# Performance work log

Hardware: AMD Instinct MI355X
Metric: run time of the kernel (lower is better)

Reference implementation:

```python
import jax, jax.numpy as jnp
import numpy as np

T = 2048
D_IN = 1024
D_OUT = 1024
N_HEAD = 16
HEAD_DIM = D_OUT // N_HEAD


def setup_inputs() -> dict:
    key = jax.random.key(0)
    kx, kq, kk, kv = jax.random.split(key, 4)
    s = 1.0 / np.sqrt(D_IN)
    return {
        "x": jax.random.normal(kx, (T, D_IN), dtype=jnp.float32),
        "W_q": jax.random.normal(kq, (D_OUT, D_IN), dtype=jnp.float32) * s,
        "W_k": jax.random.normal(kk, (D_OUT, D_IN), dtype=jnp.float32) * s,
        "W_v": jax.random.normal(kv, (D_OUT, D_IN), dtype=jnp.float32) * s,
    }


def reference(x, W_q, W_k, W_v):
    t = x.shape[0]
    # linear projections (torch Linear: y = x @ W.T), split into heads: [H, T, Dh]
    q = (x @ W_q.T).reshape(t, N_HEAD, HEAD_DIM).transpose(1, 0, 2)
    k = (x @ W_k.T).reshape(t, N_HEAD, HEAD_DIM).transpose(1, 0, 2)
    v = (x @ W_v.T).reshape(t, N_HEAD, HEAD_DIM).transpose(1, 0, 2)
    # raw scores [H, T, T]
    omega = jnp.einsum("hqd,hkd->hqk", q, k)
    causal = jnp.triu(jnp.ones((t, t), dtype=bool), k=1)
    omega = jnp.where(causal[None, :, :], -jnp.inf, omega)
    # NOTE: faithful to source quirk — divides by head_dim**(-0.5),
    # i.e. multiplies scores by sqrt(head_dim)
    att_w = jax.nn.softmax(omega * (HEAD_DIM ** 0.5), axis=-1)
    context = jnp.einsum("hqk,hkd->hqd", att_w, v)  # [H, T, Dh]
    return context.transpose(1, 0, 2).reshape(t, D_OUT)
```

## Files before the change

### kernel.cpp

```cpp
#include <hip/hip_runtime.h>
#include <hip/hip_bf16.h>


typedef __bf16 bf16x8 __attribute__((ext_vector_type(8)));
typedef __bf16 bf16x4 __attribute__((ext_vector_type(4)));
typedef float  f32x4  __attribute__((ext_vector_type(4)));
typedef float  f32x16 __attribute__((ext_vector_type(16)));
typedef unsigned int u32;
typedef u32 u32x2 __attribute__((ext_vector_type(2)));
typedef u32 u32x4 __attribute__((ext_vector_type(4)));

#define MFMA(a, b, c) __builtin_amdgcn_mfma_f32_16x16x32_bf16((a), (b), (c), 0, 0, 0)
#define MFMA32(a, b, c) __builtin_amdgcn_mfma_f32_32x32x16_bf16((a), (b), (c), 0, 0, 0)

#if __has_builtin(__builtin_amdgcn_exp2f)
#define EXP2F(x) __builtin_amdgcn_exp2f(x)
#else
#define EXP2F(x) exp2f(x)
#endif

constexpr int T = 2048, DIN = 1024, DOUT = 1024, NH = 16, DH = 64;
constexpr float SC = 11.5415603f;
constexpr float DEFER = 0.6931472f;

constexpr size_t SZ_XMAT = (size_t)T * DIN * 2;
constexpr size_t SZ_WMAT = (size_t)DOUT * DIN * 2;
constexpr size_t OFF_XH = 0;
constexpr size_t OFF_XL = OFF_XH + SZ_XMAT;
constexpr size_t OFF_QH = OFF_XL + SZ_XMAT;
constexpr size_t OFF_QL = OFF_QH + SZ_XMAT;
constexpr size_t OFF_KH = OFF_QL + SZ_XMAT;
constexpr size_t OFF_KL = OFF_KH + SZ_XMAT;
constexpr size_t OFF_VT = OFF_KL + SZ_XMAT;
constexpr size_t OFF_W  = OFF_VT + SZ_XMAT;

__device__ __forceinline__ void gload_lds16(const void* g, void* l) {
  __builtin_amdgcn_global_load_lds(
      (const __attribute__((address_space(1))) void*)g,
      (__attribute__((address_space(3))) void*)l, 16, 0, 0);
}

__device__ __forceinline__ float xor32f(float x, int hi) {
#if __has_builtin(__builtin_amdgcn_permlane32_swap)
  const u32 xu = __builtin_bit_cast(u32, x);
  const u32x2 rp = __builtin_amdgcn_permlane32_swap(xu, xu, false, false);
  return __builtin_bit_cast(float, hi ? rp[0] : rp[1]);
#else
  return __shfl_xor(x, 32, 64);
#endif
}

__global__ void split_all(const float* __restrict__ x, const float* __restrict__ wq,
                          const float* __restrict__ wk, const float* __restrict__ wv,
                          char* __restrict__ ws) {
  const int i = blockIdx.x * 256 + threadIdx.x;
  const float* src;
  __bf16 *hi, *lo;
  int off;
  if (i < T * DIN / 4) {
    src = x; off = i;
    hi = (__bf16*)(ws + OFF_XH);
    lo = (__bf16*)(ws + OFF_XL);
  } else {
    const int j = i - T * DIN / 4;
    const int z = j >> 18;
    off = j & 262143;
    src = (z == 0) ? wq : ((z == 1) ? wk : wv);
    hi = (__bf16*)(ws + OFF_W + (size_t)z * 2 * SZ_WMAT);
    lo = hi + (size_t)DOUT * DIN;
  }
  const f32x4 v = ((const f32x4*)src)[off];
  bf16x4 h, l;
#pragma unroll
  for (int j = 0; j < 4; ++j) {
    const float xv = v[j];
    const __bf16 hh = (__bf16)xv;
    h[j] = hh;
    l[j] = (__bf16)(xv - (float)hh);
  }
  ((bf16x4*)hi)[off] = h;
  ((bf16x4*)lo)[off] = l;
}

template <bool SPLIT>
__device__ __forceinline__ void proj_loop(const __bf16* __restrict__ Ah,
                                          const __bf16* __restrict__ Al,
                                          const __bf16* __restrict__ Bh,
                                          const __bf16* __restrict__ Bl,
                                          __bf16* lds, int tm, int tn, int lane,
                                          int wv, f32x4 (&acc)[4][4]) {
  constexpr int BUF = SPLIT ? 16384 : 8192;
  constexpr int BOFF = SPLIT ? 8192 : 4096;
  const int wm = wv >> 1, wn = wv & 1;
  const int q4 = lane >> 4, r16 = lane & 15;

  auto STAGE = [&](int ks, int buf) {
    const int k0 = ks * 32;
    __bf16* base = lds + buf * BUF;
#pragma unroll
    for (int j = 0; j < 2; ++j) {
      const int cbase = wv * 128 + j * 64;
      const int cidx = cbase + lane;
      const int row = cidx & 127, kc = cidx >> 7;
      const size_t ga = (size_t)(tm + row) * DIN + k0 + kc * 8;
      const size_t gb = (size_t)(tn + row) * DIN + k0 + kc * 8;
      gload_lds16(Ah + ga, base + cbase * 8);
      gload_lds16(Bh + gb, base + BOFF + cbase * 8);
      if constexpr (SPLIT) {
        gload_lds16(Al + ga, base + 4096 + cbase * 8);
        gload_lds16(Bl + gb, base + 12288 + cbase * 8);
      }
    }
  };

  STAGE(0, 0);
  STAGE(1, 1);

  for (int ks = 0; ks < 32; ++ks) {
    const int buf = ks & 1;
    if (ks < 31) {
      if constexpr (SPLIT) asm volatile("s_waitcnt vmcnt(8)" ::: "memory");
      else                 asm volatile("s_waitcnt vmcnt(4)" ::: "memory");
    } else {
      asm volatile("s_waitcnt vmcnt(0)" ::: "memory");
    }
    __builtin_amdgcn_s_barrier();
    __builtin_amdgcn_sched_barrier(0);

    const __bf16* ldsA = lds + buf * BUF;
    const __bf16* ldsB = ldsA + BOFF;

    bf16x8 fah[4], fbh[4], fal[4], fbl[4];
#pragma unroll
    for (int b = 0; b < 4; ++b) {
      const int ra = wm * 64 + b * 16 + r16;
      const int rb = wn * 64 + b * 16 + r16;
      fah[b] = *(const bf16x8*)(ldsA + (q4 * 128 + ra) * 8);
      fbh[b] = *(const bf16x8*)(ldsB + (q4 * 128 + rb) * 8);
      if constexpr (SPLIT) {
        fal[b] = *(const bf16x8*)(ldsA + 4096 + (q4 * 128 + ra) * 8);
        fbl[b] = *(const bf16x8*)(ldsB + 4096 + (q4 * 128 + rb) * 8);
      }
    }
    __builtin_amdgcn_s_setprio(1);
#pragma unroll
    for (int bm = 0; bm < 4; ++bm)
#pragma unroll
      for (int bn = 0; bn < 4; ++bn) {
        acc[bm][bn] = MFMA(fah[bm], fbh[bn], acc[bm][bn]);
        if constexpr (SPLIT) {
          acc[bm][bn] = MFMA(fah[bm], fbl[bn], acc[bm][bn]);
          acc[bm][bn] = MFMA(fal[bm], fbh[bn], acc[bm][bn]);
        }
      }
    __builtin_amdgcn_s_setprio(0);
    asm volatile("s_waitcnt lgkmcnt(0)" ::: "memory");
    __builtin_amdgcn_sched_barrier(0);
    __builtin_amdgcn_s_barrier();
    __builtin_amdgcn_sched_barrier(0);
    if (ks < 30) STAGE(ks + 2, buf);
  }
}

__global__ __launch_bounds__(256, 2) void qkv_proj(char* ws) {
  const int bid = blockIdx.x;
  const int z = bid >> 7;
  const int t_ = bid & 127;
  const int tm = (t_ >> 3) * 128;
  const int tn = (t_ & 7) * 128;
  const int tid = threadIdx.x;
  const int lane = tid & 63, wv = tid >> 6;
  const int wm = wv >> 1, wn = wv & 1;
  const int q4 = lane >> 4, r16 = lane & 15;

  const __bf16* Ah = (const __bf16*)(ws + OFF_XH);
  const __bf16* Al = (const __bf16*)(ws + OFF_XL);
  const __bf16* Bh = (const __bf16*)(ws + OFF_W + (size_t)z * 2 * SZ_WMAT);
  const __bf16* Bl = Bh + (size_t)DOUT * DIN;

  __shared__ alignas(16) __bf16 lds[32768];

  f32x4 acc[4][4] = {};

  if (z < 2) {
    proj_loop<true>(Ah, Al, Bh, Bl, lds, tm, tn, lane, wv, acc);
    __bf16* Oh = (__bf16*)(ws + (z == 0 ? OFF_QH : OFF_KH));
    __bf16* Ol = (__bf16*)(ws + (z == 0 ? OFF_QL : OFF_KL));
#pragma unroll
    for (int bm = 0; bm < 4; ++bm)
#pragma unroll
      for (int bn = 0; bn < 4; ++bn)
#pragma unroll
        for (int r = 0; r < 4; ++r) {
          const int t = tm + wm * 64 + bm * 16 + q4 * 4 + r;
          const int n = tn + wn * 64 + bn * 16 + r16;
          const float v = acc[bm][bn][r];
          const __bf16 hh = (__bf16)v;
          Oh[(size_t)t * DOUT + n] = hh;
          Ol[(size_t)t * DOUT + n] = (__bf16)(v - (float)hh);
        }
  } else {
    proj_loop<false>(Ah, Al, Bh, Bl, lds, tm, tn, lane, wv, acc);
    __syncthreads();
    __bf16* tb = lds;
#pragma unroll
    for (int bm = 0; bm < 4; ++bm)
#pragma unroll
      for (int bn = 0; bn < 4; ++bn)
#pragma unroll
        for (int r = 0; r < 4; ++r) {
          const int tl = wm * 64 + bm * 16 + q4 * 4 + r;
          const int nl = wn * 64 + bn * 16 + r16;
          tb[(size_t)nl * 136 + tl] = (__bf16)acc[bm][bn][r];
        }
    __syncthreads();
    __bf16* Vt = (__bf16*)(ws + OFF_VT);
#pragma unroll
    for (int it = 0; it < 8; ++it) {
      const int cid = it * 256 + tid;
      const int nl = cid >> 4, tc = cid & 15;
      const bf16x8 vd = *(const bf16x8*)(tb + (size_t)nl * 136 + tc * 8);
      *(bf16x8*)(Vt + (size_t)(tn + nl) * T + tm + tc * 8) = vd;
    }
  }
}

__global__ __launch_bounds__(256, 2) void attn_kernel(const char* __restrict__ ws,
                                                      float* __restrict__ out) {
  const int bid = blockIdx.x;
  const int h = bid & 15;
  const int qt = (bid < 256) ? (31 - (bid >> 4)) : ((bid - 256) >> 4);
  const int tid = threadIdx.x;
  const int lane = tid & 63, wid = tid >> 6;
  const int qhalf = wid & 1, kvpar = wid >> 1;
  const int r32 = lane & 31, hi = lane >> 5, hi8 = hi * 8;
  const int qg = qt * 64 + qhalf * 32 + r32;
  const int NT = qt + 1;
  const int mid = (NT + 1) >> 1;
  const int tBeg = kvpar ? mid : 0;
  const int tEnd = kvpar ? NT : mid;

  const __bf16* Qh = (const __bf16*)(ws + OFF_QH);
  const __bf16* Ql = (const __bf16*)(ws + OFF_QL);
  const __bf16* Kh = (const __bf16*)(ws + OFF_KH);
  const __bf16* Kl = (const __bf16*)(ws + OFF_KL);
  const __bf16* Vt = (const __bf16*)(ws + OFF_VT);

  __shared__ alignas(16) __bf16 sK[2][2][64 * 72];

  bf16x8 fqh[4], fql[4];
#pragma unroll
  for (int ds = 0; ds < 4; ++ds) {
    const size_t off = (size_t)qg * DOUT + h * 64 + ds * 16 + hi8;
    fqh[ds] = *(const bf16x8*)(Qh + off);
    fql[ds] = *(const bf16x8*)(Ql + off);
  }

  bf16x8 st[8];
  const int hid = qhalf * 64 + lane;
  auto ISSUE = [&](int t) {
    const int kv0 = t * 64;
#pragma unroll
    for (int j = 0; j < 4; ++j) {
      const int c = j * 128 + hid;
      const int row = c >> 3, dc = c & 7;
      const size_t ko = (size_t)(kv0 + row) * DOUT + h * 64 + dc * 8;
      st[j] = *(const bf16x8*)(Kh + ko);
      st[4 + j] = *(const bf16x8*)(Kl + ko);
    }
  };
  auto WRITE = [&]() {
#pragma unroll
    for (int j = 0; j < 4; ++j) {
      const int c = j * 128 + hid;
      const int row = c >> 3, dc = c & 7;
      *(bf16x8*)(&sK[kvpar][0][row * 72 + dc * 8]) = st[j];
      *(bf16x8*)(&sK[kvpar][1][row * 72 + dc * 8]) = st[4 + j];
    }
  };

  f32x16 acc0 = {}, acc1 = {};
  float mrun = -1e30f, lrun = 0.f;

  if (tBeg < tEnd) ISSUE(tBeg);

  for (int it = 0; it < mid; ++it) {
    const int t = tBeg + it;
    const bool act = (t < tEnd);
    __builtin_amdgcn_s_barrier();
    if (act) {
      WRITE();
      if (t + 1 < tEnd) ISSUE(t + 1);
    }
    asm volatile("s_waitcnt lgkmcnt(0)" ::: "memory");
    __builtin_amdgcn_sched_barrier(0);
    __builtin_amdgcn_s_barrier();
    if (!act) continue;

    const int kv0 = t * 64;
    const bool dodiag = (t == NT - 1);
    const bool do1 = !(dodiag && qhalf == 0);

    bf16x8 va0[4], va1[4];
#pragma unroll
    for (int ks = 0; ks < 4; ++ks) {
      const size_t vo = (size_t)(h * 64 + r32) * T + kv0 + ks * 16 + hi8;
      va0[ks] = *(const bf16x8*)(Vt + vo);
      va1[ks] = *(const bf16x8*)(Vt + vo + (size_t)32 * T);
    }

    const __bf16* kbh = &sK[kvpar][0][0];
    const __bf16* kbl = &sK[kvpar][1][0];
    f32x16 s0 = {}, s1 = {};
    __builtin_amdgcn_s_setprio(1);
#pragma unroll
    for (int ds = 0; ds < 4; ++ds) {
      const int ko = ds * 16 + hi8;
      const bf16x8 kh0 = *(const bf16x8*)(kbh + r32 * 72 + ko);
      const bf16x8 kl0 = *(const bf16x8*)(kbl + r32 * 72 + ko);
      s0 = MFMA32(kh0, fqh[ds], s0);
      s0 = MFMA32(kl0, fqh[ds], s0);
      s0 = MFMA32(kh0, fql[ds], s0);
    }
    if (do1) {
#pragma unroll
      for (int ds = 0; ds < 4; ++ds) {
        const int ko = ds * 16 + hi8;
        const bf16x8 kh1 = *(const bf16x8*)(kbh + (32 + r32) * 72 + ko);
        const bf16x8 kl1 = *(const bf16x8*)(kbl + (32 + r32) * 72 + ko);
        s1 = MFMA32(kh1, fqh[ds], s1);
        s1 = MFMA32(kl1, fqh[ds], s1);
        s1 = MFMA32(kh1, fql[ds], s1);
      }
    }
    __builtin_amdgcn_s_setprio(0);

    if (dodiag) {
#pragma unroll
      for (int r = 0; r < 16; ++r) {
        const int kr = (r & 3) + 8 * (r >> 2) + 4 * hi;
        if (kv0 + kr > qg) s0[r] = -1e30f;
        if (kv0 + 32 + kr > qg) s1[r] = -1e30f;
      }
    }

    float mx = -1e30f;
#pragma unroll
    for (int r = 0; r < 16; ++r) {
      mx = fmaxf(mx, s0[r]);
      mx = fmaxf(mx, s1[r]);
    }
    mx = fmaxf(mx, xor32f(mx, hi));

    if (__any(mx - mrun > DEFER)) {
      const float mnew = fmaxf(mrun, mx);
      const float scale = EXP2F((mrun - mnew) * SC);
      mrun = mnew;
      lrun *= scale;
#pragma unroll
      for (int r = 0; r < 16; ++r) {
        acc0[r] *= scale;
        acc1[r] *= scale;
      }
    }
    const float mn2 = mrun * SC;

    float ps = 0.f;
#pragma unroll
    for (int r = 0; r < 16; ++r) {
      s0[r] = EXP2F(__builtin_fmaf(s0[r], SC, -mn2));
      s1[r] = EXP2F(__builtin_fmaf(s1[r], SC, -mn2));
      ps += s0[r] + s1[r];
    }
    ps += xor32f(ps, hi);
    lrun += ps;

    bf16x8 pb[4];
#pragma unroll
    for (int ks = 0; ks < 4; ++ks) {
      const int rb = (ks & 1) * 8;
      bf16x4 lo4, hi4;
#pragma unroll
      for (int j = 0; j < 4; ++j) {
        const float pl = (ks < 2) ? s0[rb + j] : s1[rb + j];
        const float ph = (ks < 2) ? s0[rb + 4 + j] : s1[rb + 4 + j];
        lo4[j] = (__bf16)pl;
        hi4[j] = (__bf16)ph;
      }
      const u32x2 L = __builtin_bit_cast(u32x2, lo4);
      const u32x2 H = __builtin_bit_cast(u32x2, hi4);
      u32x4 f;
#if __has_builtin(__builtin_amdgcn_permlane32_swap)
#pragma unroll
      for (int q = 0; q < 2; ++q) {
        const u32x2 rp = __builtin_amdgcn_permlane32_swap(L[q], H[q], false, false);
        f[q] = rp[0];
        f[2 + q] = rp[1];
      }
#else
#pragma unroll
      for (int q = 0; q < 2; ++q) {
        const u32 send = hi ? L[q] : H[q];
        const u32 recv = (u32)__shfl_xor((int)send, 32, 64);
        f[q] = hi ? recv : L[q];
        f[2 + q] = hi ? H[q] : recv;
      }
#endif
      pb[ks] = __builtin_bit_cast(bf16x8, f);
    }

    __builtin_amdgcn_s_setprio(1);
#pragma unroll
    for (int ks = 0; ks < 4; ++ks) {
      acc0 = MFMA32(va0[ks], pb[ks], acc0);
      acc1 = MFMA32(va1[ks], pb[ks], acc1);
    }
    __builtin_amdgcn_s_setprio(0);
  }

  __builtin_amdgcn_s_barrier();
  float* mg = (float*)&sK[0][0][0];
  if (kvpar == 1) {
    float* p = mg + (qhalf * 64 + lane) * 34;
    p[0] = mrun;
    p[1] = lrun;
#pragma unroll
    for (int r = 0; r < 16; ++r) {
      p[2 + r] = acc0[r];
      p[18 + r] = acc1[r];
    }
  }
  asm volatile("s_waitcnt lgkmcnt(0)" ::: "memory");
  __builtin_amdgcn_s_barrier();
  if (kvpar == 0) {
    const float* p = mg + (qhalf * 64 + lane) * 34;
    const float m1 = p[0], l1 = p[1];
    const float M = fmaxf(mrun, m1);
    const float w0 = EXP2F((mrun - M) * SC);
    const float w1 = EXP2F((m1 - M) * SC);
    const float rl = 1.0f / (lrun * w0 + l1 * w1);
#pragma unroll
    for (int r = 0; r < 16; ++r) {
      const int d = (r & 3) + 8 * (r >> 2) + 4 * hi;
      out[(size_t)qg * DOUT + h * 64 + d] = (acc0[r] * w0 + p[2 + r] * w1) * rl;
      out[(size_t)qg * DOUT + h * 64 + 32 + d] = (acc1[r] * w0 + p[18 + r] * w1) * rl;
    }
  }
}

extern "C" void kernel_launch(void* const* d_in, const int* in_sizes, int n_in,
                              void* d_out, int out_size, void* d_ws, size_t ws_size,
                              hipStream_t stream) {
  const float* x  = (const float*)d_in[0];
  const float* Wq = (const float*)d_in[1];
  const float* Wk = (const float*)d_in[2];
  const float* Wv = (const float*)d_in[3];
  char* ws = (char*)d_ws;

  split_all<<<5120, 256, 0, stream>>>(x, Wq, Wk, Wv, ws);
  qkv_proj<<<384, 256, 0, stream>>>(ws);
  attn_kernel<<<512, 256, 0, stream>>>(ws, (float*)d_out);
}
```

Measured before the change: 96.22 us.

## Double-buffer K tiles in LDS and remap projection block order

The attention kernel now keeps two LDS buffers per KV half. The next K tile is written and the one after is prefetched while the current tile is computed, so each iteration needs one barrier instead of two and the LDS write overlaps the MFMA work. The projection kernel also permutes block indices so that consecutive block IDs are spread across the three matrices and tiles, which changes L2 locality and XCD assignment. LDS use doubles to about 73 KB for the attention block, which may reduce occupancy.

```diff
diff --git a/kernel.cpp b/kernel.cpp
--- a/kernel.cpp
+++ b/kernel.cpp
@@ -163,9 +163,9 @@
 }
 
 __global__ __launch_bounds__(256, 2) void qkv_proj(char* ws) {
-  const int bid = blockIdx.x;
-  const int z = bid >> 7;
-  const int t_ = bid & 127;
+  const int nb = (blockIdx.x & 7) * 48 + (blockIdx.x >> 3);
+  const int z = nb >> 7;
+  const int t_ = nb & 127;
   const int tm = (t_ >> 3) * 128;
   const int tn = (t_ & 7) * 128;
   const int tid = threadIdx.x;
@@ -246,7 +246,7 @@
   const __bf16* Kl = (const __bf16*)(ws + OFF_KL);
   const __bf16* Vt = (const __bf16*)(ws + OFF_VT);
 
-  __shared__ alignas(16) __bf16 sK[2][2][64 * 72];
+  __shared__ alignas(16) __bf16 sK[2][2][2][64 * 72];
 
   bf16x8 fqh[4], fql[4];
 #pragma unroll
@@ -269,157 +269,166 @@
       st[4 + j] = *(const bf16x8*)(Kl + ko);
     }
   };
-  auto WRITE = [&]() {
+  auto WRITE = [&](int b) {
 #pragma unroll
     for (int j = 0; j < 4; ++j) {
       const int c = j * 128 + hid;
       const int row = c >> 3, dc = c & 7;
-      *(bf16x8*)(&sK[kvpar][0][row * 72 + dc * 8]) = st[j];
-      *(bf16x8*)(&sK[kvpar][1][row * 72 + dc * 8]) = st[4 + j];
+      *(bf16x8*)(&sK[kvpar][b][0][row * 72 + dc * 8]) = st[j];
+      *(bf16x8*)(&sK[kvpar][b][1][row * 72 + dc * 8]) = st[4 + j];
     }
   };
 
   f32x16 acc0 = {}, acc1 = {};
   float mrun = -1e30f, lrun = 0.f;
 
-  if (tBeg < tEnd) ISSUE(tBeg);
+  if (tBeg < tEnd) {
+    ISSUE(tBeg);
+    WRITE(0);
+    if (tBeg + 1 < tEnd) ISSUE(tBeg + 1);
+  }
+  asm volatile("s_waitcnt lgkmcnt(0)" ::: "memory");
+  __builtin_amdgcn_sched_barrier(0);
+  __builtin_amdgcn_s_barrier();
+  __builtin_amdgcn_sched_barrier(0);
 
   for (int it = 0; it < mid; ++it) {
     const int t = tBeg + it;
-    const bool act = (t < tEnd);
-    __builtin_amdgcn_s_barrier();
-    if (act) {
-      WRITE();
-      if (t + 1 < tEnd) ISSUE(t + 1);
-    }
+    const int p = it & 1;
+    if (t < tEnd) {
+      if (t + 1 < tEnd) {
+        WRITE(p ^ 1);
+        if (t + 2 < tEnd) ISSUE(t + 2);
+      }
+
+      const int kv0 = t * 64;
+      const bool dodiag = (t == NT - 1);
+      const bool do1 = !(dodiag && qhalf == 0);
+
+      bf16x8 va0[4], va1[4];
+#pragma unroll
+      for (int ks = 0; ks < 4; ++ks) {
+        const size_t vo = (size_t)(h * 64 + r32) * T + kv0 + ks * 16 + hi8;
+        va0[ks] = *(const bf16x8*)(Vt + vo);
+        va1[ks] = *(const bf16x8*)(Vt + vo + (size_t)32 * T);
+      }
+
+      const __bf16* kbh = &sK[kvpar][p][0][0];
+      const __bf16* kbl = &sK[kvpar][p][1][0];
+      f32x16 s0 = {}, s1 = {};
+      __builtin_amdgcn_s_setprio(1);
+#pragma unroll
+      for (int ds = 0; ds < 4; ++ds) {
+        const int ko = ds * 16 + hi8;
+        const bf16x8 kh0 = *(const bf16x8*)(kbh + r32 * 72 + ko);
+        const bf16x8 kl0 = *(const bf16x8*)(kbl + r32 * 72 + ko);
+        s0 = MFMA32(kh0, fqh[ds], s0);
+        s0 = MFMA32(kl0, fqh[ds], s0);
+        s0 = MFMA32(kh0, fql[ds], s0);
+      }
+      if (do1) {
+#pragma unroll
+        for (int ds = 0; ds < 4; ++ds) {
+          const int ko = ds * 16 + hi8;
+          const bf16x8 kh1 = *(const bf16x8*)(kbh + (32 + r32) * 72 + ko);
+          const bf16x8 kl1 = *(const bf16x8*)(kbl + (32 + r32) * 72 + ko);
+          s1 = MFMA32(kh1, fqh[ds], s1);
+          s1 = MFMA32(kl1, fqh[ds], s1);
+          s1 = MFMA32(kh1, fql[ds], s1);
+        }
+      }
+      __builtin_amdgcn_s_setprio(0);
+
+      if (dodiag) {
+#pragma unroll
+        for (int r = 0; r < 16; ++r) {
+          const int kr = (r & 3) + 8 * (r >> 2) + 4 * hi;
+          if (kv0 + kr > qg) s0[r] = -1e30f;
+          if (kv0 + 32 + kr > qg) s1[r] = -1e30f;
+        }
+      }
+
+      float mx = -1e30f;
+#pragma unroll
+      for (int r = 0; r < 16; ++r) {
+        mx = fmaxf(mx, s0[r]);
+        mx = fmaxf(mx, s1[r]);
+      }
+      mx = fmaxf(mx, xor32f(mx, hi));
+
+      if (__any(mx - mrun > DEFER)) {
+        const float mnew = fmaxf(mrun, mx);
+        const float scale = EXP2F((mrun - mnew) * SC);
+        mrun = mnew;
+        lrun *= scale;
+#pragma unroll
+        for (int r = 0; r < 16; ++r) {
+          acc0[r] *= scale;
+          acc1[r] *= scale;
+        }
+      }
+      const float mn2 = mrun * SC;
+
+      float ps = 0.f;
+#pragma unroll
+      for (int r = 0; r < 16; ++r) {
+        s0[r] = EXP2F(__builtin_fmaf(s0[r], SC, -mn2));
+        s1[r] = EXP2F(__builtin_fmaf(s1[r], SC, -mn2));
+        ps += s0[r] + s1[r];
+      }
+      ps += xor32f(ps, hi);
+      lrun += ps;
+
+      bf16x8 pb[4];
+#pragma unroll
+      for (int ks = 0; ks < 4; ++ks) {
+        const int rb = (ks & 1) * 8;
+        bf16x4 lo4, hi4;
+#pragma unroll
+        for (int j = 0; j < 4; ++j) {
+          const float pl = (ks < 2) ? s0[rb + j] : s1[rb + j];
+          const float ph = (ks < 2) ? s0[rb + 4 + j] : s1[rb + 4 + j];
+          lo4[j] = (__bf16)pl;
+          hi4[j] = (__bf16)ph;
+        }
+        const u32x2 L = __builtin_bit_cast(u32x2, lo4);
+        const u32x2 H = __builtin_bit_cast(u32x2, hi4);
+        u32x4 f;
+#if __has_builtin(__builtin_amdgcn_permlane32_swap)
+#pragma unroll
+        for (int q = 0; q < 2; ++q) {
+          const u32x2 rp = __builtin_amdgcn_permlane32_swap(L[q], H[q], false, false);
+          f[q] = rp[0];
+          f[2 + q] = rp[1];
+        }
+#else
+#pragma unroll
+        for (int q = 0; q < 2; ++q) {
+          const u32 send = hi ? L[q] : H[q];
+          const u32 recv = (u32)__shfl_xor((int)send, 32, 64);
+          f[q] = hi ? recv : L[q];
+          f[2 + q] = hi ? H[q] : recv;
+        }
+#endif
+        pb[ks] = __builtin_bit_cast(bf16x8, f);
+      }
+
+      __builtin_amdgcn_s_setprio(1);
+#pragma unroll
+      for (int ks = 0; ks < 4; ++ks) {
+        acc0 = MFMA32(va0[ks], pb[ks], acc0);
+        acc1 = MFMA32(va1[ks], pb[ks], acc1);
+      }
+      __builtin_amdgcn_s_setprio(0);
+    }
+
     asm volatile("s_waitcnt lgkmcnt(0)" ::: "memory");
     __builtin_amdgcn_sched_barrier(0);
     __builtin_amdgcn_s_barrier();
-    if (!act) continue;
-
-    const int kv0 = t * 64;
-    const bool dodiag = (t == NT - 1);
-    const bool do1 = !(dodiag && qhalf == 0);
-
-    bf16x8 va0[4], va1[4];
-#pragma unroll
-    for (int ks = 0; ks < 4; ++ks) {
-      const size_t vo = (size_t)(h * 64 + r32) * T + kv0 + ks * 16 + hi8;
-      va0[ks] = *(const bf16x8*)(Vt + vo);
-      va1[ks] = *(const bf16x8*)(Vt + vo + (size_t)32 * T);
-    }
-
-    const __bf16* kbh = &sK[kvpar][0][0];
-    const __bf16* kbl = &sK[kvpar][1][0];
-    f32x16 s0 = {}, s1 = {};
-    __builtin_amdgcn_s_setprio(1);
-#pragma unroll
-    for (int ds = 0; ds < 4; ++ds) {
-      const int ko = ds * 16 + hi8;
-      const bf16x8 kh0 = *(const bf16x8*)(kbh + r32 * 72 + ko);
-      const bf16x8 kl0 = *(const bf16x8*)(kbl + r32 * 72 + ko);
-      s0 = MFMA32(kh0, fqh[ds], s0);
-      s0 = MFMA32(kl0, fqh[ds], s0);
-      s0 = MFMA32(kh0, fql[ds], s0);
-    }
-    if (do1) {
-#pragma unroll
-      for (int ds = 0; ds < 4; ++ds) {
-        const int ko = ds * 16 + hi8;
-        const bf16x8 kh1 = *(const bf16x8*)(kbh + (32 + r32) * 72 + ko);
-        const bf16x8 kl1 = *(const bf16x8*)(kbl + (32 + r32) * 72 + ko);
-        s1 = MFMA32(kh1, fqh[ds], s1);
-        s1 = MFMA32(kl1, fqh[ds], s1);
-        s1 = MFMA32(kh1, fql[ds], s1);
-      }
-    }
-    __builtin_amdgcn_s_setprio(0);
-
-    if (dodiag) {
-#pragma unroll
-      for (int r = 0; r < 16; ++r) {
-        const int kr = (r & 3) + 8 * (r >> 2) + 4 * hi;
-        if (kv0 + kr > qg) s0[r] = -1e30f;
-        if (kv0 + 32 + kr > qg) s1[r] = -1e30f;
-      }
-    }
-
-    float mx = -1e30f;
-#pragma unroll
-    for (int r = 0; r < 16; ++r) {
-      mx = fmaxf(mx, s0[r]);
-      mx = fmaxf(mx, s1[r]);
-    }
-    mx = fmaxf(mx, xor32f(mx, hi));
-
-    if (__any(mx - mrun > DEFER)) {
-      const float mnew = fmaxf(mrun, mx);
-      const float scale = EXP2F((mrun - mnew) * SC);
-      mrun = mnew;
-      lrun *= scale;
-#pragma unroll
-      for (int r = 0; r < 16; ++r) {
-        acc0[r] *= scale;
-        acc1[r] *= scale;
-      }
-    }
-    const float mn2 = mrun * SC;
-
-    float ps = 0.f;
-#pragma unroll
-    for (int r = 0; r < 16; ++r) {
-      s0[r] = EXP2F(__builtin_fmaf(s0[r], SC, -mn2));
-      s1[r] = EXP2F(__builtin_fmaf(s1[r], SC, -mn2));
-      ps += s0[r] + s1[r];
-    }
-    ps += xor32f(ps, hi);
-    lrun += ps;
-
-    bf16x8 pb[4];
-#pragma unroll
-    for (int ks = 0; ks < 4; ++ks) {
-      const int rb = (ks & 1) * 8;
-      bf16x4 lo4, hi4;
-#pragma unroll
-      for (int j = 0; j < 4; ++j) {
-        const float pl = (ks < 2) ? s0[rb + j] : s1[rb + j];
-        const float ph = (ks < 2) ? s0[rb + 4 + j] : s1[rb + 4 + j];
-        lo4[j] = (__bf16)pl;
-        hi4[j] = (__bf16)ph;
-      }
-      const u32x2 L = __builtin_bit_cast(u32x2, lo4);
-      const u32x2 H = __builtin_bit_cast(u32x2, hi4);
-      u32x4 f;
-#if __has_builtin(__builtin_amdgcn_permlane32_swap)
-#pragma unroll
-      for (int q = 0; q < 2; ++q) {
-        const u32x2 rp = __builtin_amdgcn_permlane32_swap(L[q], H[q], false, false);
-        f[q] = rp[0];
-        f[2 + q] = rp[1];
-      }
-#else
-#pragma unroll
-      for (int q = 0; q < 2; ++q) {
-        const u32 send = hi ? L[q] : H[q];
-        const u32 recv = (u32)__shfl_xor((int)send, 32, 64);
-        f[q] = hi ? recv : L[q];
-        f[2 + q] = hi ? H[q] : recv;
-      }
-#endif
-      pb[ks] = __builtin_bit_cast(bf16x8, f);
-    }
-
-    __builtin_amdgcn_s_setprio(1);
-#pragma unroll
-    for (int ks = 0; ks < 4; ++ks) {
-      acc0 = MFMA32(va0[ks], pb[ks], acc0);
-      acc1 = MFMA32(va1[ks], pb[ks], acc1);
-    }
-    __builtin_amdgcn_s_setprio(0);
-  }
-
-  __builtin_amdgcn_s_barrier();
-  float* mg = (float*)&sK[0][0][0];
+    __builtin_amdgcn_sched_barrier(0);
+  }
+
+  float* mg = (float*)&sK[0][0][0][0];
   if (kvpar == 1) {
     float* p = mg + (qhalf * 64 + lane) * 34;
     p[0] = mrun;
```

Result: slower. 112.4 us (+16.8%).
